# Kernel tuning notes

Hardware: AMD Instinct MI355X
Metric: run time of the kernel (lower is better)

Reference implementation:

```python
import jax, jax.numpy as jnp
import numpy as np

N, T, F, H, DEG = 1024, 32, 128, 4, 32
HID, OUT = 512, 64
NNZ = N * DEG
D = F // H


def setup_inputs() -> dict:
    key = jax.random.key(0)
    ks = jax.random.split(key, 40)
    p = lambda i, shape, s=0.05: (jax.random.normal(ks[i], shape, dtype=jnp.float32) * s)
    inp = {
        'A_rows': jnp.repeat(jnp.arange(N, dtype=jnp.int32), DEG),
        'A_cols': jax.random.randint(ks[0], (NNZ,), 0, N, dtype=jnp.int32),
        'A_vals': jax.random.uniform(ks[1], (NNZ,), dtype=jnp.float32) / DEG,
        'X': jax.random.normal(ks[2], (N, T, F), dtype=jnp.float32),
        'W_gcn': p(3, (F, F)),
        'W_ih': p(4, (3 * F, F)), 'W_hh': p(5, (3 * F, F)),
        'b_ih': p(6, (3 * F,)), 'b_hh': p(7, (3 * F,)),
        'in_proj_w': p(8, (3 * F, F)), 'in_proj_b': p(9, (3 * F,)),
        'out_proj_w': p(10, (F, F)), 'out_proj_b': p(11, (F,)),
        'ln1_g': jnp.ones((F,), jnp.float32), 'ln1_b': jnp.zeros((F,), jnp.float32),
        'ln2_g': jnp.ones((F,), jnp.float32), 'ln2_b': jnp.zeros((F,), jnp.float32),
        'lnf_g': jnp.ones((F,), jnp.float32), 'lnf_b': jnp.zeros((F,), jnp.float32),
        'ff1_w': p(12, (HID, F)), 'ff1_b': p(13, (HID,)),
        'ff2_w': p(14, (F, HID)), 'ff2_b': p(15, (F,)),
        'fc1_w': p(16, (HID, T * F)), 'fc1_b': p(17, (HID,)),
        'fc2_w': p(18, (HID, HID)), 'fc2_b': p(19, (HID,)),
        'fc3_w': p(20, (OUT, HID)), 'fc3_b': p(21, (OUT,)),
    }
    return inp


def _pos_encoding():
    # pe[i, t] = sin(t / 10000**(2i/F)) for even t, cos(...) for odd t; constant over feature dim.
    i = jnp.arange(N, dtype=jnp.float32)
    t = jnp.arange(T, dtype=jnp.float32)
    inv = jnp.exp(-(2.0 * i / F) * jnp.log(jnp.float32(10000.0)))  # [N]
    ang = t[None, :] * inv[:, None]                                # [N, T]
    even = (jnp.arange(T) % 2 == 0)[None, :]
    return jnp.where(even, jnp.sin(ang), jnp.cos(ang))             # [N, T]


def _layer_norm(x, g, b, eps=1e-5):
    mu = x.mean(-1, keepdims=True)
    var = ((x - mu) ** 2).mean(-1, keepdims=True)
    return (x - mu) * jax.lax.rsqrt(var + eps) * g + b


def _forward(A_rows, A_cols, A_vals, X, W_gcn, W_ih, W_hh, b_ih, b_hh,
             in_proj_w, in_proj_b, out_proj_w, out_proj_b,
             ln1_g, ln1_b, ln2_g, ln2_b, lnf_g, lnf_b,
             ff1_w, ff1_b, ff2_w, ff2_b,
             fc1_w, fc1_b, fc2_w, fc2_b, fc3_w, fc3_b):
    def spmm(x2d):  # A_hat @ x2d via COO gather + segment-sum
        return jax.ops.segment_sum(A_vals[:, None] * x2d[A_cols], A_rows, num_segments=N)

    def gru_cell(x, h):  # torch GRUCell, gate order [r; z; n]
        gi = x @ W_ih.T + b_ih
        gh = h @ W_hh.T + b_hh
        ir, iz, inn = jnp.split(gi, 3, axis=-1)
        hr, hz, hn = jnp.split(gh, 3, axis=-1)
        r = jax.nn.sigmoid(ir + hr)
        z = jax.nn.sigmoid(iz + hz)
        n = jnp.tanh(inn + r * hn)
        return (1.0 - z) * n + z * h

    # GCN on full [N, T, F] block
    X_tilde = jax.nn.relu(spmm(X.reshape(N, T * F)).reshape(N, T, F) @ W_gcn)

    # sequential GRU + per-step GCN over time
    def step(h, x_t):
        g = gru_cell(x_t, h)                       # [N, F]
        h_new = jax.nn.relu(spmm(g) @ W_gcn)
        return h_new, g

    h0 = jnp.zeros((N, F), X.dtype)
    _, Hs = jax.lax.scan(step, h0, jnp.transpose(X_tilde, (1, 0, 2)))  # [T, N, F]
    Hm = jnp.transpose(Hs, (1, 0, 2)) + _pos_encoding()[:, :, None]    # [N, T, F]

    # TransformerEncoderLayer (post-norm, relu, dropout=0); seq axis = nodes, batch axis = T
    qkv = Hm @ in_proj_w.T + in_proj_b                 # [N, T, 3F]
    q, k, v = jnp.split(qkv, 3, axis=-1)
    q = q.reshape(N, T, H, D) * (1.0 / jnp.sqrt(jnp.float32(D)))
    k = k.reshape(N, T, H, D)
    v = v.reshape(N, T, H, D)
    scores = jnp.einsum('nthd,mthd->thnm', q, k)       # [T, H, N, N]
    attn = jax.nn.softmax(scores, axis=-1)
    ctx = jnp.einsum('thnm,mthd->nthd', attn, v).reshape(N, T, F)
    attn_out = ctx @ out_proj_w.T + out_proj_b
    x1 = _layer_norm(Hm + attn_out, ln1_g, ln1_b)
    ff = jax.nn.relu(x1 @ ff1_w.T + ff1_b) @ ff2_w.T + ff2_b
    x2 = _layer_norm(x1 + ff, ln2_g, ln2_b)
    enc = _layer_norm(x2, lnf_g, lnf_b)                # final encoder norm

    # MLP head
    flat = enc.reshape(N, T * F)
    h1 = jax.nn.relu(flat @ fc1_w.T + fc1_b)
    h2 = jax.nn.relu(h1 @ fc2_w.T + fc2_b)
    return h2 @ fc3_w.T + fc3_b                        # [N, OUT]


def reference(A_rows, A_cols, A_vals, X, W_gcn, W_ih, W_hh, b_ih, b_hh,
              in_proj_w, in_proj_b, out_proj_w, out_proj_b,
              ln1_g, ln1_b, ln2_g, ln2_b, lnf_g, lnf_b,
              ff1_w, ff1_b, ff2_w, ff2_b,
              fc1_w, fc1_b, fc2_w, fc2_b, fc3_w, fc3_b):
    return _forward(A_rows, A_cols, A_vals, X, W_gcn, W_ih, W_hh, b_ih, b_hh,
                    in_proj_w, in_proj_b, out_proj_w, out_proj_b,
                    ln1_g, ln1_b, ln2_g, ln2_b, lnf_g, lnf_b,
                    ff1_w, ff1_b, ff2_w, ff2_b,
                    fc1_w, fc1_b, fc2_w, fc2_b, fc3_w, fc3_b)
```

## Files before the change

### kernel.cpp

```cpp
#include <hip/hip_runtime.h>
#include <hip/hip_bf16.h>
#include <math.h>

#define N_NODES 1024
#define T_STEPS 32
#define F_DIM   128
#define H_HEADS 4
#define D_HEAD  32
#define DEG     32
#define HID     512
#define OUT_DIM 64
#define TF      (T_STEPS * F_DIM)
#define NT      (N_NODES * T_STEPS)
#define F3      (3 * F_DIM)

typedef __attribute__((ext_vector_type(8))) __bf16 bf16x8;
typedef __attribute__((ext_vector_type(4))) float  f32x4;

__device__ __forceinline__ short f2bf(float x) {
    union { float f; unsigned u; } v; v.f = x;
    unsigned r = (v.u + 0x7FFFu + ((v.u >> 16) & 1u)) >> 16;
    return (short)r;
}
__device__ __forceinline__ float bf2f(unsigned short b) {
    union { unsigned u; float f; } v; v.u = ((unsigned)b) << 16; return v.f;
}

__global__ void zero_kernel(float* p, int n) {
    int i = blockIdx.x * 256 + threadIdx.x;
    if (i < n) p[i] = 0.f;
}

template <bool RELU>
__global__ void bias_act(float* __restrict__ C, const float* __restrict__ bias,
                         int P, int total) {
    int i = blockIdx.x * 256 + threadIdx.x;
    if (i < total) {
        float v = C[i] + bias[i & (P - 1)];
        if (RELU) v = fmaxf(v, 0.f);
        C[i] = v;
    }
}

__global__ void prep_weights(const float* __restrict__ W_hh, const float* __restrict__ W_gcn,
                             unsigned short* __restrict__ WhhT_bf,
                             unsigned short* __restrict__ Wg_bf) {
    int idx = blockIdx.x * 256 + threadIdx.x;
    if (idx < F3 * F_DIM) {
        int j = idx / F_DIM;
        int k = idx % F_DIM;
        WhhT_bf[k * F3 + j] = (unsigned short)f2bf(W_hh[idx]);
    }
    if (idx < F_DIM * F_DIM) {
        Wg_bf[idx] = (unsigned short)f2bf(W_gcn[idx]);
    }
}

__global__ void spmm_wide(const int* __restrict__ cols, const float* __restrict__ vals,
                          const float* __restrict__ X, float* __restrict__ Y) {
    int n = blockIdx.y;
    int c = blockIdx.x * 256 + threadIdx.x;
    const int*   ce = cols + n * DEG;
    const float* ve = vals + n * DEG;
    float acc = 0.f;
#pragma unroll
    for (int e = 0; e < DEG; ++e) acc += ve[e] * X[ce[e] * TF + c];
    Y[n * TF + c] = acc;
}

__global__ __launch_bounds__(256) void gates0_kernel(
        const float* __restrict__ GI, const float* __restrict__ b_hh,
        float* __restrict__ g_out, float* __restrict__ Hm) {
    int idx = blockIdx.x * 256 + threadIdx.x;
    int n = idx >> 7, f = idx & 127;
    size_t gib = (size_t)n * T_STEPS * F3;
    float rr = 1.f / (1.f + expf(-(GI[gib + f] + b_hh[f])));
    float zz = 1.f / (1.f + expf(-(GI[gib + 128 + f] + b_hh[128 + f])));
    float nn = tanhf(GI[gib + 256 + f] + rr * b_hh[256 + f]);
    float g  = (1.f - zz) * nn;
    g_out[idx] = g;
    Hm[(size_t)n * T_STEPS * F_DIM + f] = g;
}

__global__ __launch_bounds__(256) void scan_step(
        const int* __restrict__ cols, const float* __restrict__ vals,
        const float* __restrict__ g_in, const unsigned short* __restrict__ Wg_bf,
        const unsigned short* __restrict__ WhhT_bf, const float* __restrict__ b_hh,
        const float* __restrict__ GI, float* __restrict__ g_out,
        float* __restrict__ Hm, int t_next) {
    __shared__ float sp[4][F_DIM];
    __shared__ float hsn[4][F_DIM];
    __shared__ float part[2][F_DIM][13];
    __shared__ float gpart[2][4][F_DIM];
    int tid = threadIdx.x;
    int n0 = blockIdx.x * 4;
    int f = tid & 127, half = tid >> 7;
    float b4[4] = {0.f, 0.f, 0.f, 0.f};
    int eb = half * 16;
#pragma unroll
    for (int j = 0; j < 4; ++j) {
#pragma unroll
        for (int e = 0; e < 16; ++e) {
            int idx = (n0 + j) * DEG + eb + e;
            b4[j] += vals[idx] * g_in[cols[idx] * F_DIM + f];
        }
    }
#pragma unroll
    for (int j = 0; j < 4; ++j) gpart[half][j][f] = b4[j];
    __syncthreads();
    for (int idx = tid; idx < 512; idx += 256) {
        int j = idx >> 7, ff = idx & 127;
        sp[j][ff] = gpart[0][j][ff] + gpart[1][j][ff];
    }
    __syncthreads();
    int kb = half * 64;
    float c4[4] = {0.f, 0.f, 0.f, 0.f};
#pragma unroll 4
    for (int k = 0; k < 64; ++k) {
        int kk = kb + k;
        float w = bf2f(Wg_bf[kk * F_DIM + f]);
        c4[0] += sp[0][kk] * w; c4[1] += sp[1][kk] * w;
        c4[2] += sp[2][kk] * w; c4[3] += sp[3][kk] * w;
    }
#pragma unroll
    for (int j = 0; j < 4; ++j) gpart[half][j][f] = c4[j];
    __syncthreads();
    for (int idx = tid; idx < 512; idx += 256) {
        int j = idx >> 7, ff = idx & 127;
        hsn[j][ff] = fmaxf(gpart[0][j][ff] + gpart[1][j][ff], 0.f);
    }
    __syncthreads();
    float a[12];
#pragma unroll
    for (int i = 0; i < 12; ++i) a[i] = 0.f;
#pragma unroll 2
    for (int k = 0; k < 64; ++k) {
        int kk = kb + k;
        const unsigned short* w = WhhT_bf + kk * F3;
        float wr = bf2f(w[f]), wz = bf2f(w[128 + f]), wn = bf2f(w[256 + f]);
        float h0 = hsn[0][kk], h1 = hsn[1][kk], h2 = hsn[2][kk], h3 = hsn[3][kk];
        a[0] += h0 * wr; a[1]  += h0 * wz; a[2]  += h0 * wn;
        a[3] += h1 * wr; a[4]  += h1 * wz; a[5]  += h1 * wn;
        a[6] += h2 * wr; a[7]  += h2 * wz; a[8]  += h2 * wn;
        a[9] += h3 * wr; a[10] += h3 * wz; a[11] += h3 * wn;
    }
#pragma unroll
    for (int i = 0; i < 12; ++i) part[half][f][i] = a[i];
    __syncthreads();
#pragma unroll
    for (int jj = 0; jj < 2; ++jj) {
        int j = half * 2 + jj;
        int node = n0 + j;
        float ghr = part[0][f][j * 3 + 0] + part[1][f][j * 3 + 0] + b_hh[f];
        float ghz = part[0][f][j * 3 + 1] + part[1][f][j * 3 + 1] + b_hh[128 + f];
        float ghn = part[0][f][j * 3 + 2] + part[1][f][j * 3 + 2] + b_hh[256 + f];
        size_t gib = ((size_t)node * T_STEPS + t_next) * F3;
        float hv = hsn[j][f];
        float rr = 1.f / (1.f + expf(-(GI[gib + f] + ghr)));
        float zz = 1.f / (1.f + expf(-(GI[gib + 128 + f] + ghz)));
        float nn = tanhf(GI[gib + 256 + f] + rr * ghn);
        float g  = (1.f - zz) * nn + zz * hv;
        g_out[node * F_DIM + f] = g;
        float inv = __expf(-(float)node * (9.210340371976184f / 64.0f));
        float ang = (float)t_next * inv;
        float pe  = ((t_next & 1) == 0) ? sinf(ang) : cosf(ang);
        Hm[((size_t)node * T_STEPS + t_next) * F_DIM + f] = g + pe;
    }
}

__global__ __launch_bounds__(256) void qkv_gemm(const float* __restrict__ A,
                                                const float* __restrict__ B,
                                                const float* __restrict__ bias,
                                                short* __restrict__ Qb,
                                                short* __restrict__ Kb,
                                                short* __restrict__ VTb) {
    __shared__ short As[64][40];
    __shared__ short Bs[64][40];
    int tid = threadIdx.x;
    int p0 = blockIdx.x * 64, row0 = blockIdx.y * 64;
    int lane = tid & 63, w = tid >> 6, col = lane & 15, quad = lane >> 4;
    f32x4 acc[4];
#pragma unroll
    for (int j = 0; j < 4; ++j) acc[j] = (f32x4){0.f, 0.f, 0.f, 0.f};
    for (int k0 = 0; k0 < F_DIM; k0 += 32) {
#pragma unroll
        for (int i = 0; i < 2; ++i) {
            int idx = tid * 2 + i;
            int r = idx >> 3, c4 = (idx & 7) << 2;
            const float4 f4 = *(const float4*)(A + (size_t)(row0 + r) * F_DIM + k0 + c4);
            union { __hip_bfloat162 h2[2]; short4 s4; } u;
            u.h2[0] = __float22bfloat162_rn(make_float2(f4.x, f4.y));
            u.h2[1] = __float22bfloat162_rn(make_float2(f4.z, f4.w));
            *(short4*)&As[r][c4] = u.s4;
        }
#pragma unroll
        for (int i = 0; i < 2; ++i) {
            int idx = tid * 2 + i;
            int r = idx >> 3, c4 = (idx & 7) << 2;
            const float4 f4 = *(const float4*)(B + (size_t)(p0 + r) * F_DIM + k0 + c4);
            union { __hip_bfloat162 h2[2]; short4 s4; } u;
            u.h2[0] = __float22bfloat162_rn(make_float2(f4.x, f4.y));
            u.h2[1] = __float22bfloat162_rn(make_float2(f4.z, f4.w));
            *(short4*)&Bs[r][c4] = u.s4;
        }
        __syncthreads();
        bf16x8 af = *(const bf16x8*)&As[w * 16 + col][quad * 8];
#pragma unroll
        for (int j = 0; j < 4; ++j) {
            bf16x8 bv = *(const bf16x8*)&Bs[j * 16 + col][quad * 8];
            acc[j] = __builtin_amdgcn_mfma_f32_16x16x32_bf16(af, bv, acc[j], 0, 0, 0);
        }
        __syncthreads();
    }
#pragma unroll
    for (int j = 0; j < 4; ++j) {
        int cg = p0 + j * 16 + col;
        int which = cg >> 7, f = cg & 127;
        int hh = f >> 5, d = f & 31;
        float bv = bias[cg];
#pragma unroll
        for (int r = 0; r < 4; ++r) {
            int rg = row0 + w * 16 + quad * 4 + r;
            int n = rg >> 5, t = rg & 31;
            int th = t * H_HEADS + hh;
            float v = acc[j][r] + bv;
            if (which == 0)
                Qb[((size_t)th * N_NODES + n) * D_HEAD + d] = f2bf(v * 0.17677669529663687f);
            else if (which == 1)
                Kb[((size_t)th * N_NODES + n) * D_HEAD + d] = f2bf(v);
            else
                VTb[((size_t)th * D_HEAD + d) * N_NODES + n] = f2bf(v);
        }
    }
}

__global__ __launch_bounds__(64) void attn_mfma(const short* __restrict__ Qb,
                                                const short* __restrict__ Kb,
                                                const short* __restrict__ VTb,
                                                float* __restrict__ ctx) {
    int th = blockIdx.x;
    int t = th >> 2, hh = th & 3;
    int q0 = blockIdx.y * 16;
    int lane = threadIdx.x;
    int col  = lane & 15;
    int quad = lane >> 4;
    __shared__ short Ps[16][40];

    bf16x8 qf = *(const bf16x8*)(Qb + ((size_t)(th * N_NODES + q0 + col)) * D_HEAD + quad * 8);
    const short* Kbase = Kb  + (size_t)th * (N_NODES * D_HEAD);
    const short* Vbase = VTb + (size_t)th * (D_HEAD * N_NODES);

    f32x4 o0 = {0.f, 0.f, 0.f, 0.f}, o1 = {0.f, 0.f, 0.f, 0.f};
    float lr0 = 0.f, lr1 = 0.f, lr2 = 0.f, lr3 = 0.f;
    const f32x4 zc = {0.f, 0.f, 0.f, 0.f};

    for (int mt = 0; mt < 32; ++mt) {
        int m0 = mt * 32;
        bf16x8 k0 = *(const bf16x8*)(Kbase + (size_t)(m0 + col) * D_HEAD + quad * 8);
        bf16x8 k1 = *(const bf16x8*)(Kbase + (size_t)(m0 + 16 + col) * D_HEAD + quad * 8);
        f32x4 s0 = __builtin_amdgcn_mfma_f32_16x16x32_bf16(qf, k0, zc, 0, 0, 0);
        f32x4 s1 = __builtin_amdgcn_mfma_f32_16x16x32_bf16(qf, k1, zc, 0, 0, 0);
        float p0[4], p1[4];
#pragma unroll
        for (int r = 0; r < 4; ++r) {
            p0[r] = __expf(fminf(s0[r], 80.f));
            p1[r] = __expf(fminf(s1[r], 80.f));
        }
        lr0 += p0[0] + p1[0]; lr1 += p0[1] + p1[1];
        lr2 += p0[2] + p1[2]; lr3 += p0[3] + p1[3];
        __syncthreads();
#pragma unroll
        for (int r = 0; r < 4; ++r) {
            union { __hip_bfloat162 h; short2 s; } u;
            u.h = __float22bfloat162_rn(make_float2(p0[r], p1[r]));
            Ps[quad * 4 + r][col]      = u.s.x;
            Ps[quad * 4 + r][col + 16] = u.s.y;
        }
        __syncthreads();
        bf16x8 pf = *(const bf16x8*)(&Ps[col][quad * 8]);
        bf16x8 v0 = *(const bf16x8*)(Vbase + (size_t)col * N_NODES + m0 + quad * 8);
        bf16x8 v1 = *(const bf16x8*)(Vbase + (size_t)(col + 16) * N_NODES + m0 + quad * 8);
        o0 = __builtin_amdgcn_mfma_f32_16x16x32_bf16(pf, v0, o0, 0, 0, 0);
        o1 = __builtin_amdgcn_mfma_f32_16x16x32_bf16(pf, v1, o1, 0, 0, 0);
    }
    float lr[4] = {lr0, lr1, lr2, lr3};
#pragma unroll
    for (int r = 0; r < 4; ++r) {
        float s = lr[r];
        s += __shfl_xor(s, 1); s += __shfl_xor(s, 2);
        s += __shfl_xor(s, 4); s += __shfl_xor(s, 8);
        lr[r] = 1.f / s;
    }
#pragma unroll
    for (int r = 0; r < 4; ++r) {
        int n = q0 + quad * 4 + r;
        size_t base = ((size_t)n * T_STEPS + t) * F_DIM + hh * D_HEAD;
        ctx[base + col]      = o0[r] * lr[r];
        ctx[base + 16 + col] = o1[r] * lr[r];
    }
}

__global__ __launch_bounds__(256) void ln_kernel(
        const float* __restrict__ a, const float* __restrict__ resid,
        const float* __restrict__ gamma, const float* __restrict__ beta,
        float* __restrict__ out) {
    int row = blockIdx.x * 4 + (threadIdx.x >> 6);
    int tid = threadIdx.x & 63;
    int base = row * F_DIM;
    float x0 = a[base + tid], x1 = a[base + 64 + tid];
    if (resid) { x0 += resid[base + tid]; x1 += resid[base + 64 + tid]; }
    float s = x0 + x1;
#pragma unroll
    for (int o = 32; o > 0; o >>= 1) s += __shfl_xor(s, o);
    float mu = s * (1.f / 128.f);
    float d0 = x0 - mu, d1 = x1 - mu;
    float v = d0 * d0 + d1 * d1;
#pragma unroll
    for (int o = 32; o > 0; o >>= 1) v += __shfl_xor(v, o);
    float inv = rsqrtf(v * (1.f / 128.f) + 1e-5f);
    out[base + tid]      = d0 * inv * gamma[tid] + beta[tid];
    out[base + 64 + tid] = d1 * inv * gamma[64 + tid] + beta[64 + tid];
}

template <bool TB, bool RELU, bool SPLITK>
__global__ __launch_bounds__(256) void mfma_gemm(const float* __restrict__ A,
                                                 const float* __restrict__ B,
                                                 const float* __restrict__ bias,
                                                 float* __restrict__ C,
                                                 int M, int K, int P, int Kc) {
    __shared__ short As[64][40];
    __shared__ short Bs[64][40];
    int tid = threadIdx.x;
    int p0 = blockIdx.x * 64, row0 = blockIdx.y * 64;
    int k_begin = SPLITK ? blockIdx.z * Kc : 0;
    int k_end   = SPLITK ? k_begin + Kc : K;
    int lane = tid & 63, w = tid >> 6, col = lane & 15, quad = lane >> 4;
    f32x4 acc[4];
#pragma unroll
    for (int j = 0; j < 4; ++j) acc[j] = (f32x4){0.f, 0.f, 0.f, 0.f};

    for (int k0 = k_begin; k0 < k_end; k0 += 32) {
#pragma unroll
        for (int i = 0; i < 2; ++i) {
            int idx = tid * 2 + i;
            int r = idx >> 3, c4 = (idx & 7) << 2;
            const float4 f4 = *(const float4*)(A + (size_t)(row0 + r) * K + k0 + c4);
            union { __hip_bfloat162 h2[2]; short4 s4; } u;
            u.h2[0] = __float22bfloat162_rn(make_float2(f4.x, f4.y));
            u.h2[1] = __float22bfloat162_rn(make_float2(f4.z, f4.w));
            *(short4*)&As[r][c4] = u.s4;
        }
        if (TB) {
#pragma unroll
            for (int i = 0; i < 2; ++i) {
                int idx = tid * 2 + i;
                int r = idx >> 3, c4 = (idx & 7) << 2;
                const float4 f4 = *(const float4*)(B + (size_t)(p0 + r) * K + k0 + c4);
                union { __hip_bfloat162 h2[2]; short4 s4; } u;
                u.h2[0] = __float22bfloat162_rn(make_float2(f4.x, f4.y));
                u.h2[1] = __float22bfloat162_rn(make_float2(f4.z, f4.w));
                *(short4*)&Bs[r][c4] = u.s4;
            }
        } else {
#pragma unroll
            for (int i = 0; i < 2; ++i) {
                int idx = tid * 2 + i;
                int kk = idx >> 4, c4 = (idx & 15) << 2;
                const float4 f4 = *(const float4*)(B + (size_t)(k0 + kk) * P + p0 + c4);
                Bs[c4 + 0][kk] = f2bf(f4.x);
                Bs[c4 + 1][kk] = f2bf(f4.y);
                Bs[c4 + 2][kk] = f2bf(f4.z);
                Bs[c4 + 3][kk] = f2bf(f4.w);
            }
        }
        __syncthreads();
        bf16x8 af = *(const bf16x8*)&As[w * 16 + col][quad * 8];
#pragma unroll
        for (int j = 0; j < 4; ++j) {
            bf16x8 bv = *(const bf16x8*)&Bs[j * 16 + col][quad * 8];
            acc[j] = __builtin_amdgcn_mfma_f32_16x16x32_bf16(af, bv, acc[j], 0, 0, 0);
        }
        __syncthreads();
    }
#pragma unroll
    for (int j = 0; j < 4; ++j) {
        int cg_ = p0 + j * 16 + col;
        float bvv = (!SPLITK && bias) ? bias[cg_] : 0.f;
#pragma unroll
        for (int r = 0; r < 4; ++r) {
            int rg = row0 + w * 16 + quad * 4 + r;
            if (SPLITK) {
                atomicAdd(&C[(size_t)rg * P + cg_], acc[j][r]);
            } else {
                float v = acc[j][r] + bvv;
                if (RELU) v = fmaxf(v, 0.f);
                C[(size_t)rg * P + cg_] = v;
            }
        }
    }
}

extern "C" void kernel_launch(void* const* d_in, const int* in_sizes, int n_in,
                              void* d_out, int out_size, void* d_ws, size_t ws_size,
                              hipStream_t stream) {
    const int*   A_cols     = (const int*)d_in[1];
    const float* A_vals     = (const float*)d_in[2];
    const float* X          = (const float*)d_in[3];
    const float* W_gcn      = (const float*)d_in[4];
    const float* W_ih       = (const float*)d_in[5];
    const float* W_hh       = (const float*)d_in[6];
    const float* b_ih       = (const float*)d_in[7];
    const float* b_hh       = (const float*)d_in[8];
    const float* in_proj_w  = (const float*)d_in[9];
    const float* in_proj_b  = (const float*)d_in[10];
    const float* out_proj_w = (const float*)d_in[11];
    const float* out_proj_b = (const float*)d_in[12];
    const float* ln1_g = (const float*)d_in[13];
    const float* ln1_b = (const float*)d_in[14];
    const float* ln2_g = (const float*)d_in[15];
    const float* ln2_b = (const float*)d_in[16];
    const float* lnf_g = (const float*)d_in[17];
    const float* lnf_b = (const float*)d_in[18];
    const float* ff1_w = (const float*)d_in[19];
    const float* ff1_b = (const float*)d_in[20];
    const float* ff2_w = (const float*)d_in[21];
    const float* ff2_b = (const float*)d_in[22];
    const float* fc1_w = (const float*)d_in[23];
    const float* fc1_b = (const float*)d_in[24];
    const float* fc2_w = (const float*)d_in[25];
    const float* fc2_b = (const float*)d_in[26];
    const float* fc3_w = (const float*)d_in[27];
    const float* fc3_b = (const float*)d_in[28];
    float* out = (float*)d_out;
    float* ws  = (float*)d_ws;

    const size_t o_Hm = 0;
    const size_t o_A  = o_Hm + 4194304;
    const size_t o_B  = o_A + 4194304;
    const size_t o_C  = o_B + 4194304;
    const size_t o_D  = o_C + 12582912;
    const size_t o_WT = o_D + 12582912;
    const size_t o_h  = o_WT + 49152;
    const size_t o_g  = o_h + 131072;
    const size_t o_h1 = o_g + 131072;
    const size_t o_h2 = o_h1 + 524288;

    float* Hm    = ws + o_Hm;
    float* bufA  = ws + o_A;
    float* bufB  = ws + o_B;
    float* bufC  = ws + o_C;
    short* Qb    = (short*)(ws + o_D);
    short* Kb    = Qb + 4194304;
    short* VTb   = Kb + 4194304;
    unsigned short* WhhT_bf = (unsigned short*)(ws + o_WT);
    unsigned short* Wg_bf   = WhhT_bf + 49152;
    float* g0    = ws + o_g;
    float* h1    = ws + o_h1;
    float* h2    = ws + o_h2;
    float* g1    = h2;

    spmm_wide<<<dim3(16, 1024), 256, 0, stream>>>(A_cols, A_vals, X, bufA);
    mfma_gemm<false, true, false><<<dim3(2, 512), 256, 0, stream>>>(bufA, W_gcn, nullptr, bufB, NT, F_DIM, F_DIM, 0);
    mfma_gemm<true, false, false><<<dim3(6, 512), 256, 0, stream>>>(bufB, W_ih, b_ih, bufC, NT, F_DIM, F3, 0);
    prep_weights<<<192, 256, 0, stream>>>(W_hh, W_gcn, WhhT_bf, Wg_bf);
    gates0_kernel<<<512, 256, 0, stream>>>(bufC, b_hh, g0, Hm);
    for (int s = 0; s < T_STEPS - 1; ++s) {
        const float* gi = (s & 1) ? g1 : g0;
        float*       go = (s & 1) ? g0 : g1;
        scan_step<<<256, 256, 0, stream>>>(A_cols, A_vals, gi, Wg_bf, WhhT_bf, b_hh, bufC, go, Hm, s + 1);
    }
    qkv_gemm<<<dim3(6, 512), 256, 0, stream>>>(Hm, in_proj_w, in_proj_b, Qb, Kb, VTb);
    attn_mfma<<<dim3(128, 64), 64, 0, stream>>>(Qb, Kb, VTb, bufA);
    mfma_gemm<true, false, false><<<dim3(2, 512), 256, 0, stream>>>(bufA, out_proj_w, out_proj_b, bufB, NT, F_DIM, F_DIM, 0);
    ln_kernel<<<NT / 4, 256, 0, stream>>>(Hm, bufB, ln1_g, ln1_b, bufA);
    mfma_gemm<true, true, false><<<dim3(8, 512), 256, 0, stream>>>(bufA, ff1_w, ff1_b, bufC, NT, F_DIM, HID, 0);
    mfma_gemm<true, false, false><<<dim3(2, 512), 256, 0, stream>>>(bufC, ff2_w, ff2_b, bufB, NT, HID, F_DIM, 0);
    ln_kernel<<<NT / 4, 256, 0, stream>>>(bufA, bufB, ln2_g, ln2_b, Hm);
    ln_kernel<<<NT / 4, 256, 0, stream>>>(Hm, nullptr, lnf_g, lnf_b, bufA);
    zero_kernel<<<2048, 256, 0, stream>>>(h1, 524288);
    mfma_gemm<true, false, true><<<dim3(8, 16, 4), 256, 0, stream>>>(bufA, fc1_w, nullptr, h1, N_NODES, TF, HID, 1024);
    bias_act<true><<<2048, 256, 0, stream>>>(h1, fc1_b, HID, 524288);
    zero_kernel<<<2048, 256, 0, stream>>>(h2, 524288);
    mfma_gemm<true, false, true><<<dim3(8, 16, 4), 256, 0, stream>>>(h1, fc2_w, nullptr, h2, N_NODES, HID, HID, 128);
    bias_act<true><<<2048, 256, 0, stream>>>(h2, fc2_b, HID, 524288);
    zero_kernel<<<256, 256, 0, stream>>>(out, 65536);
    mfma_gemm<true, false, true><<<dim3(1, 16, 8), 256, 0, stream>>>(h2, fc3_w, nullptr, out, N_NODES, HID, OUT_DIM, 64);
    bias_act<false><<<256, 256, 0, stream>>>(out, fc3_b, OUT_DIM, 65536);
}
```

Measured before the change: 869.9 us.

## Share K/V tiles across four waves in attention; halve nodes per scan block

Result: faster. 775.0 us (-10.9%).

```diff
diff --git a/kernel.cpp b/kernel.cpp
--- a/kernel.cpp
+++ b/kernel.cpp
@@ -88,74 +88,58 @@
         const unsigned short* __restrict__ WhhT_bf, const float* __restrict__ b_hh,
         const float* __restrict__ GI, float* __restrict__ g_out,
         float* __restrict__ Hm, int t_next) {
-    __shared__ float sp[4][F_DIM];
-    __shared__ float hsn[4][F_DIM];
-    __shared__ float part[2][F_DIM][13];
-    __shared__ float gpart[2][4][F_DIM];
+    __shared__ float sp[2][F_DIM];
+    __shared__ float hsn[2][F_DIM];
+    __shared__ float part[2][F_DIM][8];
+    __shared__ float gpart[2][2][F_DIM];
     int tid = threadIdx.x;
-    int n0 = blockIdx.x * 4;
+    int n0 = blockIdx.x * 2;
     int f = tid & 127, half = tid >> 7;
-    float b4[4] = {0.f, 0.f, 0.f, 0.f};
+    float b0 = 0.f, b1 = 0.f;
     int eb = half * 16;
 #pragma unroll
-    for (int j = 0; j < 4; ++j) {
-#pragma unroll
-        for (int e = 0; e < 16; ++e) {
-            int idx = (n0 + j) * DEG + eb + e;
-            b4[j] += vals[idx] * g_in[cols[idx] * F_DIM + f];
-        }
-    }
-#pragma unroll
-    for (int j = 0; j < 4; ++j) gpart[half][j][f] = b4[j];
+    for (int e = 0; e < 16; ++e) {
+        int i0 = n0 * DEG + eb + e;
+        int i1 = (n0 + 1) * DEG + eb + e;
+        b0 += vals[i0] * g_in[cols[i0] * F_DIM + f];
+        b1 += vals[i1] * g_in[cols[i1] * F_DIM + f];
+    }
+    gpart[half][0][f] = b0; gpart[half][1][f] = b1;
     __syncthreads();
-    for (int idx = tid; idx < 512; idx += 256) {
-        int j = idx >> 7, ff = idx & 127;
-        sp[j][ff] = gpart[0][j][ff] + gpart[1][j][ff];
-    }
+    sp[half][f] = gpart[0][half][f] + gpart[1][half][f];
     __syncthreads();
+    float c0 = 0.f, c1 = 0.f;
     int kb = half * 64;
-    float c4[4] = {0.f, 0.f, 0.f, 0.f};
 #pragma unroll 4
     for (int k = 0; k < 64; ++k) {
         int kk = kb + k;
         float w = bf2f(Wg_bf[kk * F_DIM + f]);
-        c4[0] += sp[0][kk] * w; c4[1] += sp[1][kk] * w;
-        c4[2] += sp[2][kk] * w; c4[3] += sp[3][kk] * w;
-    }
-#pragma unroll
-    for (int j = 0; j < 4; ++j) gpart[half][j][f] = c4[j];
+        c0 += sp[0][kk] * w; c1 += sp[1][kk] * w;
+    }
+    gpart[half][0][f] = c0; gpart[half][1][f] = c1;
     __syncthreads();
-    for (int idx = tid; idx < 512; idx += 256) {
-        int j = idx >> 7, ff = idx & 127;
-        hsn[j][ff] = fmaxf(gpart[0][j][ff] + gpart[1][j][ff], 0.f);
-    }
+    hsn[half][f] = fmaxf(gpart[0][half][f] + gpart[1][half][f], 0.f);
     __syncthreads();
-    float a[12];
-#pragma unroll
-    for (int i = 0; i < 12; ++i) a[i] = 0.f;
+    float a[6] = {0.f, 0.f, 0.f, 0.f, 0.f, 0.f};
 #pragma unroll 2
     for (int k = 0; k < 64; ++k) {
         int kk = kb + k;
         const unsigned short* w = WhhT_bf + kk * F3;
         float wr = bf2f(w[f]), wz = bf2f(w[128 + f]), wn = bf2f(w[256 + f]);
-        float h0 = hsn[0][kk], h1 = hsn[1][kk], h2 = hsn[2][kk], h3 = hsn[3][kk];
-        a[0] += h0 * wr; a[1]  += h0 * wz; a[2]  += h0 * wn;
-        a[3] += h1 * wr; a[4]  += h1 * wz; a[5]  += h1 * wn;
-        a[6] += h2 * wr; a[7]  += h2 * wz; a[8]  += h2 * wn;
-        a[9] += h3 * wr; a[10] += h3 * wz; a[11] += h3 * wn;
-    }
-#pragma unroll
-    for (int i = 0; i < 12; ++i) part[half][f][i] = a[i];
+        float h0 = hsn[0][kk], h1 = hsn[1][kk];
+        a[0] += h0 * wr; a[1] += h0 * wz; a[2] += h0 * wn;
+        a[3] += h1 * wr; a[4] += h1 * wz; a[5] += h1 * wn;
+    }
+#pragma unroll
+    for (int i = 0; i < 6; ++i) part[half][f][i] = a[i];
     __syncthreads();
-#pragma unroll
-    for (int jj = 0; jj < 2; ++jj) {
-        int j = half * 2 + jj;
-        int node = n0 + j;
-        float ghr = part[0][f][j * 3 + 0] + part[1][f][j * 3 + 0] + b_hh[f];
-        float ghz = part[0][f][j * 3 + 1] + part[1][f][j * 3 + 1] + b_hh[128 + f];
-        float ghn = part[0][f][j * 3 + 2] + part[1][f][j * 3 + 2] + b_hh[256 + f];
+    {
+        int node = n0 + half;
+        float ghr = part[0][f][half * 3 + 0] + part[1][f][half * 3 + 0] + b_hh[f];
+        float ghz = part[0][f][half * 3 + 1] + part[1][f][half * 3 + 1] + b_hh[128 + f];
+        float ghn = part[0][f][half * 3 + 2] + part[1][f][half * 3 + 2] + b_hh[256 + f];
         size_t gib = ((size_t)node * T_STEPS + t_next) * F3;
-        float hv = hsn[j][f];
+        float hv = hsn[half][f];
         float rr = 1.f / (1.f + expf(-(GI[gib + f] + ghr)));
         float zz = 1.f / (1.f + expf(-(GI[gib + 128 + f] + ghz)));
         float nn = tanhf(GI[gib + 256 + f] + rr * ghn);
@@ -234,56 +218,61 @@
     }
 }
 
-__global__ __launch_bounds__(64) void attn_mfma(const short* __restrict__ Qb,
-                                                const short* __restrict__ Kb,
-                                                const short* __restrict__ VTb,
-                                                float* __restrict__ ctx) {
+__global__ __launch_bounds__(256) void attn_mfma(const short* __restrict__ Qb,
+                                                 const short* __restrict__ Kb,
+                                                 const short* __restrict__ VTb,
+                                                 float* __restrict__ ctx) {
     int th = blockIdx.x;
     int t = th >> 2, hh = th & 3;
-    int q0 = blockIdx.y * 16;
-    int lane = threadIdx.x;
-    int col  = lane & 15;
-    int quad = lane >> 4;
-    __shared__ short Ps[16][40];
-
-    bf16x8 qf = *(const bf16x8*)(Qb + ((size_t)(th * N_NODES + q0 + col)) * D_HEAD + quad * 8);
+    int q0 = blockIdx.y * 64;
+    int tid = threadIdx.x;
+    int w = tid >> 6, lane = tid & 63;
+    int col = lane & 15, quad = lane >> 4;
+    __shared__ short    Ks[32][40];
+    __shared__ short    Vs[32][40];
+    __shared__ unsigned Ps[4][16][20];
+
+    bf16x8 qf = *(const bf16x8*)(Qb + ((size_t)th * N_NODES + q0 + w * 16 + col) * D_HEAD + quad * 8);
     const short* Kbase = Kb  + (size_t)th * (N_NODES * D_HEAD);
     const short* Vbase = VTb + (size_t)th * (D_HEAD * N_NODES);
 
+    int lrw = tid >> 3;
+    int lc  = (tid & 7) * 4;
+    int kperm = ((lrw & 15) << 1) | (lrw >> 4);
+
     f32x4 o0 = {0.f, 0.f, 0.f, 0.f}, o1 = {0.f, 0.f, 0.f, 0.f};
-    float lr0 = 0.f, lr1 = 0.f, lr2 = 0.f, lr3 = 0.f;
+    float l0 = 0.f, l1 = 0.f, l2 = 0.f, l3 = 0.f;
     const f32x4 zc = {0.f, 0.f, 0.f, 0.f};
 
     for (int mt = 0; mt < 32; ++mt) {
         int m0 = mt * 32;
-        bf16x8 k0 = *(const bf16x8*)(Kbase + (size_t)(m0 + col) * D_HEAD + quad * 8);
-        bf16x8 k1 = *(const bf16x8*)(Kbase + (size_t)(m0 + 16 + col) * D_HEAD + quad * 8);
+        __syncthreads();
+        *(short4*)&Ks[lrw][lc] = *(const short4*)(Kbase + (size_t)(m0 + kperm) * D_HEAD + lc);
+        *(short4*)&Vs[lrw][lc] = *(const short4*)(Vbase + (size_t)lrw * N_NODES + m0 + lc);
+        __syncthreads();
+        bf16x8 k0 = *(const bf16x8*)&Ks[col][quad * 8];
+        bf16x8 k1 = *(const bf16x8*)&Ks[col + 16][quad * 8];
         f32x4 s0 = __builtin_amdgcn_mfma_f32_16x16x32_bf16(qf, k0, zc, 0, 0, 0);
         f32x4 s1 = __builtin_amdgcn_mfma_f32_16x16x32_bf16(qf, k1, zc, 0, 0, 0);
-        float p0[4], p1[4];
+        float ps[4][2];
 #pragma unroll
         for (int r = 0; r < 4; ++r) {
-            p0[r] = __expf(fminf(s0[r], 80.f));
-            p1[r] = __expf(fminf(s1[r], 80.f));
-        }
-        lr0 += p0[0] + p1[0]; lr1 += p0[1] + p1[1];
-        lr2 += p0[2] + p1[2]; lr3 += p0[3] + p1[3];
-        __syncthreads();
-#pragma unroll
-        for (int r = 0; r < 4; ++r) {
-            union { __hip_bfloat162 h; short2 s; } u;
-            u.h = __float22bfloat162_rn(make_float2(p0[r], p1[r]));
-            Ps[quad * 4 + r][col]      = u.s.x;
-            Ps[quad * 4 + r][col + 16] = u.s.y;
-        }
-        __syncthreads();
-        bf16x8 pf = *(const bf16x8*)(&Ps[col][quad * 8]);
-        bf16x8 v0 = *(const bf16x8*)(Vbase + (size_t)col * N_NODES + m0 + quad * 8);
-        bf16x8 v1 = *(const bf16x8*)(Vbase + (size_t)(col + 16) * N_NODES + m0 + quad * 8);
+            ps[r][0] = __expf(fminf(s0[r], 80.f));
+            ps[r][1] = __expf(fminf(s1[r], 80.f));
+            union { __hip_bfloat162 h; unsigned u; } u;
+            u.h = __float22bfloat162_rn(make_float2(ps[r][0], ps[r][1]));
+            Ps[w][quad * 4 + r][col] = u.u;
+        }
+        l0 += ps[0][0] + ps[0][1]; l1 += ps[1][0] + ps[1][1];
+        l2 += ps[2][0] + ps[2][1]; l3 += ps[3][0] + ps[3][1];
+        __builtin_amdgcn_s_waitcnt(0xC07F);
+        bf16x8 pf = *(const bf16x8*)&Ps[w][col][quad * 4];
+        bf16x8 v0 = *(const bf16x8*)&Vs[col][quad * 8];
+        bf16x8 v1 = *(const bf16x8*)&Vs[col + 16][quad * 8];
         o0 = __builtin_amdgcn_mfma_f32_16x16x32_bf16(pf, v0, o0, 0, 0, 0);
         o1 = __builtin_amdgcn_mfma_f32_16x16x32_bf16(pf, v1, o1, 0, 0, 0);
     }
-    float lr[4] = {lr0, lr1, lr2, lr3};
+    float lr[4] = {l0, l1, l2, l3};
 #pragma unroll
     for (int r = 0; r < 4; ++r) {
         float s = lr[r];
@@ -293,7 +282,7 @@
     }
 #pragma unroll
     for (int r = 0; r < 4; ++r) {
-        int n = q0 + quad * 4 + r;
+        int n = q0 + w * 16 + quad * 4 + r;
         size_t base = ((size_t)n * T_STEPS + t) * F_DIM + hh * D_HEAD;
         ctx[base + col]      = o0[r] * lr[r];
         ctx[base + 16 + col] = o1[r] * lr[r];
@@ -467,10 +456,10 @@
     for (int s = 0; s < T_STEPS - 1; ++s) {
         const float* gi = (s & 1) ? g1 : g0;
         float*       go = (s & 1) ? g0 : g1;
-        scan_step<<<256, 256, 0, stream>>>(A_cols, A_vals, gi, Wg_bf, WhhT_bf, b_hh, bufC, go, Hm, s + 1);
+        scan_step<<<512, 256, 0, stream>>>(A_cols, A_vals, gi, Wg_bf, WhhT_bf, b_hh, bufC, go, Hm, s + 1);
     }
     qkv_gemm<<<dim3(6, 512), 256, 0, stream>>>(Hm, in_proj_w, in_proj_b, Qb, Kb, VTb);
-    attn_mfma<<<dim3(128, 64), 64, 0, stream>>>(Qb, Kb, VTb, bufA);
+    attn_mfma<<<dim3(128, 16), 256, 0, stream>>>(Qb, Kb, VTb, bufA);
     mfma_gemm<true, false, false><<<dim3(2, 512), 256, 0, stream>>>(bufA, out_proj_w, out_proj_b, bufB, NT, F_DIM, F_DIM, 0);
     ln_kernel<<<NT / 4, 256, 0, stream>>>(Hm, bufB, ln1_g, ln1_b, bufA);
     mfma_gemm<true, true, false><<<dim3(8, 512), 256, 0, stream>>>(bufA, ff1_w, ff1_b, bufC, NT, F_DIM, HID, 0);
```
